# Optimization experiments

Hardware: AMD Instinct MI355X
Metric: run time of the kernel (lower is better)

The kernel has to match this reference:

```python
import jax, jax.numpy as jnp
import numpy as np
import math

FS = 9          # gaussian filter_size
STD = 1.0
LOW = 0.1       # min(threshold1, threshold2)
HIGH = 0.3      # max(threshold1, threshold2)
PAD_G = FS // 2


def _gauss_window(M, std):
    # scipy.signal.windows.gaussian: exp(-0.5*(n/std)^2), n centered, unnormalized
    n = np.arange(M, dtype=np.float64) - (M - 1) / 2.0
    return np.exp(-0.5 * (n / std) ** 2).astype(np.float32)


def _conv(x, w, pad):
    # torch F.conv2d == cross-correlation, NCHW / OIHW
    return jax.lax.conv_general_dilated(
        x, w, window_strides=(1, 1), padding=pad,
        dimension_numbers=("NCHW", "OIHW", "NCHW"))


def setup_inputs() -> dict:
    key = jax.random.key(0)
    img = jax.random.uniform(key, (8, 3, 512, 512), dtype=jnp.float32)
    g = _gauss_window(FS, STD)
    gauss_h = jnp.asarray(g[None, None, None, :])          # [1,1,1,9]
    gauss_v = jnp.asarray(g[None, None, :, None])          # [1,1,9,1]
    sobel_h = jnp.array([[[[1., 0., -1.], [2., 0., -2.], [1., 0., -1.]]]], dtype=jnp.float32)
    sobel_v = jnp.array([[[[1., 2., 1.], [0., 0., 0.], [-1., -2., -1.]]]], dtype=jnp.float32)
    d = np.zeros((8, 1, 3, 3), dtype=np.float32)
    d[:, 0, 1, 1] = 1.0
    # neighbor positions (row, col) for the -1 tap, per directional channel
    neigh = [(1, 2), (2, 2), (2, 1), (2, 0), (1, 0), (0, 0), (0, 1), (0, 2)]
    for k, (r, c) in enumerate(neigh):
        d[k, 0, r, c] = -1.0
    directional = jnp.asarray(d)                            # [8,1,3,3]
    connect = jnp.array([[[[1., 1., 1.], [1., 0., 1.], [1., 1., 1.]]]], dtype=jnp.float32)
    return {"img": img, "gauss_h": gauss_h, "gauss_v": gauss_v,
            "sobel_h": sobel_h, "sobel_v": sobel_v,
            "directional": directional, "connect": connect}


def reference(img, gauss_h, gauss_v, sobel_h, sobel_v, directional, connect):
    B, C, H, W = img.shape
    x = img.reshape(B * C, 1, H, W)  # per-channel 1-in/1-out convs, batched
    blur = _conv(_conv(x, gauss_h, [(0, 0), (PAD_G, PAD_G)]),
                 gauss_v, [(PAD_G, PAD_G), (0, 0)])
    gx = _conv(blur, sobel_h, [(1, 1), (1, 1)]).reshape(B, C, H, W)
    gy = _conv(blur, sobel_v, [(1, 1), (1, 1)]).reshape(B, C, H, W)

    # sum of per-channel magnitudes, [B,1,H,W]
    grad_mag = jnp.sqrt(gx * gx + gy * gy).sum(axis=1, keepdims=True)
    ori = jnp.arctan2(gy.sum(axis=1, keepdims=True),
                      gx.sum(axis=1, keepdims=True)) * (180.0 / math.pi) + 180.0
    ori = jnp.round(ori / 45.0) * 45.0

    all_filtered = _conv(grad_mag, directional, [(1, 1), (1, 1)])  # [B,8,H,W]

    pixel_count = B * H * W
    pr = jnp.arange(pixel_count, dtype=jnp.int32)
    flat = all_filtered.reshape(-1)
    # faithful replication of the original's flat linear-index gather
    k_pos = ((ori / 45.0) % 8.0).reshape(-1).astype(jnp.int32)
    k_neg = ((ori / 45.0 + 4.0) % 8.0).reshape(-1).astype(jnp.int32)
    pos = flat[k_pos * pixel_count + pr].reshape(B, 1, H, W)
    neg = flat[k_neg * pixel_count + pr].reshape(B, 1, H, W)

    is_max = jnp.minimum(pos, neg) > 0.0
    thin = jnp.where(is_max, grad_mag, 0.0)

    t = jnp.where(thin < LOW, 0.0, thin)
    higher = thin > HIGH
    t = jnp.where(higher, 1.0, t)
    connect_map = _conv(higher.astype(jnp.float32), connect, [(1, 1), (1, 1)])
    middle = (thin >= LOW) & (thin <= HIGH)
    t = jnp.where(middle, 0.0, t)
    connect_map = jnp.where(middle, connect_map, 0.0)
    t = jnp.where(connect_map > 0.0, 1.0, t)
    # zero borders
    t = t.at[..., 0, :].set(0.0)
    t = t.at[..., -1, :].set(0.0)
    t = t.at[..., :, 0].set(0.0)
    t = t.at[..., :, -1].set(0.0)
    return (t > 0.0).astype(jnp.float32)
```

## Files before the change

kernel.cpp:

```cpp
#include <hip/hip_runtime.h>
#include <math.h>

#define HH 512
#define WW 512
#define NB 8
#define NC 3
#define HW (HH*WW)

#define RSTRIP 16
#define CSTRIP 62
#define NROWS (HH/RSTRIP)
#define NCOLS ((WW + CSTRIP - 1)/CSTRIP)
#define WPB 2

__global__ __launch_bounds__(128) void canny_gm_kernel(
    const float* __restrict__ img, const float* __restrict__ gwin,
    float* __restrict__ GM, unsigned char* __restrict__ KP)
{
    const int lane = threadIdx.x & 63;
    const int wv   = threadIdx.x >> 6;
    const int cs   = blockIdx.x % NCOLS;
    const int rs   = (blockIdx.x / NCOLS) * WPB + wv;
    const int b    = blockIdx.y;

    const int R0 = rs * RSTRIP;
    const int cl = cs * CSTRIP - 1 + lane;

    double g[9];
#pragma unroll
    for (int k = 0; k < 9; ++k) g[k] = (double)gwin[k];

    int cidx[9]; double gk[9];
#pragma unroll
    for (int k = 0; k < 9; ++k) {
        int cc = cl - 4 + k;
        bool m = ((unsigned)cc < (unsigned)WW);
        gk[k] = m ? g[k] : 0.0;
        int cc2 = cc < 0 ? 0 : cc;
        cidx[k] = cc2 > (WW - 1) ? (WW - 1) : cc2;
    }
    const bool lane_out = (lane >= 1) && (lane <= CSTRIP) && (cl < WW);
    const bool cml = ((unsigned)(cl - 1) < (unsigned)WW);
    const bool cmr = ((unsigned)(cl + 1) < (unsigned)WW);

    const float* ip0 = img + ((size_t)b * NC + 0) * HW;
    const float* ip1 = img + ((size_t)b * NC + 1) * HW;
    const float* ip2 = img + ((size_t)b * NC + 2) * HW;

    double hb[3][9];
    double vb[3][3];
#pragma unroll
    for (int c = 0; c < 3; ++c) {
#pragma unroll
        for (int k = 0; k < 9; ++k) hb[c][k] = 0.0;
#pragma unroll
        for (int k = 0; k < 3; ++k) vb[c][k] = 0.0;
    }

    const double t225 = 0.41421356237309503;
    const double t675 = 2.414213562373095;

    auto PHASE = [&](int r, int ph, bool doV, bool doS) {
        if ((unsigned)r < (unsigned)HH) {
            const size_t ro = (size_t)r * WW;
            float v0[9], v1[9], v2[9];
#pragma unroll
            for (int k = 0; k < 9; ++k) {
                v0[k] = ip0[ro + cidx[k]];
                v1[k] = ip1[ro + cidx[k]];
                v2[k] = ip2[ro + cidx[k]];
            }
            double a0 = 0.0, a1 = 0.0, a2 = 0.0;
#pragma unroll
            for (int k = 0; k < 9; ++k) {
                a0 = fma(gk[k], (double)v0[k], a0);
                a1 = fma(gk[k], (double)v1[k], a1);
                a2 = fma(gk[k], (double)v2[k], a2);
            }
            hb[0][ph] = a0; hb[1][ph] = a1; hb[2][ph] = a2;
        } else {
            hb[0][ph] = 0.0; hb[1][ph] = 0.0; hb[2][ph] = 0.0;
        }

        if (doV) {
#pragma unroll
            for (int c = 0; c < 3; ++c) {
                double acc = 0.0;
#pragma unroll
                for (int k = 0; k < 9; ++k)
                    acc = fma(g[k], hb[c][(ph + 1 + k) % 9], acc);
                vb[c][(ph + 2) % 3] = acc;
            }
        }

        if (doS) {
            const int ri = r - 5;
            const bool up = (ri >= 1), dn = (ri <= HH - 2);
            double mag = 0.0, sgx = 0.0, sgy = 0.0;
#pragma unroll
            for (int c = 0; c < 3; ++c) {
                double top = up ? vb[c][ph % 3]       : 0.0;
                double mid =      vb[c][(ph + 1) % 3];
                double bot = dn ? vb[c][(ph + 2) % 3] : 0.0;
                double s = top + 2.0 * mid + bot;
                double d = top - bot;
                double sL = __shfl_up(s, 1), sR = __shfl_down(s, 1);
                double dL = __shfl_up(d, 1), dR = __shfl_down(d, 1);
                sL = cml ? sL : 0.0;  sR = cmr ? sR : 0.0;
                dL = cml ? dL : 0.0;  dR = cmr ? dR : 0.0;
                double gx = sL - sR;
                double gy = dL + 2.0 * d + dR;
                mag += sqrt(gx * gx + gy * gy);
                sgx += gx; sgy += gy;
            }
            if (lane_out) {
                size_t o = (size_t)b * HW + (size_t)ri * WW + cl;
                GM[o] = (float)mag;
                double ax = fabs(sgx), ay = fabs(sgy);
                int kp;
                if (ay <= ax * t225)      kp = (sgx >= 0.0) ? 4 : 0;
                else if (ay >= ax * t675) kp = (sgy > 0.0) ? 6 : 2;
                else if (sgx > 0.0)       kp = (sgy > 0.0) ? 5 : 3;
                else                      kp = (sgy > 0.0) ? 7 : 1;
                KP[o] = (unsigned char)kp;
            }
        }
    };

    {
        const int rb = R0 - 5;
#pragma unroll
        for (int ph = 0; ph < 9; ++ph) PHASE(rb + ph, ph, ph == 8, false);
    }
    {
        const int rb = R0 + 4;
#pragma unroll
        for (int ph = 0; ph < 9; ++ph) PHASE(rb + ph, ph, true, ph >= 1);
    }
    {
        const int rb = R0 + 13;
#pragma unroll
        for (int ph = 0; ph < 8; ++ph) PHASE(rb + ph, ph, true, true);
    }
}

__global__ __launch_bounds__(256) void canny_thin_out_kernel(
    const float* __restrict__ GM, const unsigned char* __restrict__ KP,
    float* __restrict__ out)
{
    __shared__ unsigned char scode[34 * 35];

    const int tilesX = WW / 32;
    const int tx0 = (blockIdx.x % tilesX) * 32;
    const int ty0 = (blockIdx.x / tilesX) * 32;
    const int b = blockIdx.y;
    const int t = threadIdx.x;

    const int dr = (int)((0x00012221u >> (b * 4)) & 15u) - 1;
    const int dc = (int)((0x21000122u >> (b * 4)) & 15u) - 1;

    {
        int r = t / 34, cc = t % 34, idx = t;
#pragma unroll
        for (int it = 0; it < 5; ++it) {
            if (idx < 34 * 34) {
                int gi = ty0 - 1 + r, gj = tx0 - 1 + cc;
                unsigned char code = 0;
                if ((unsigned)gi < (unsigned)HH && (unsigned)gj < (unsigned)WW) {
                    size_t p0 = (size_t)gi * WW + gj;
                    int kp = KP[(size_t)b * HW + p0];
                    int kn = (kp + 4) & 7;
                    int ni = gi + dr, nj = gj + dc;
                    bool nin = ((unsigned)ni < (unsigned)HH) && ((unsigned)nj < (unsigned)WW);
                    size_t pn = (size_t)ni * WW + nj;
                    double gmp  = (double)GM[(size_t)kp * HW + p0];
                    double gmn  = (double)GM[(size_t)kn * HW + p0];
                    double gmpn = nin ? (double)GM[(size_t)kp * HW + pn] : 0.0;
                    double gmnn = nin ? (double)GM[(size_t)kn * HW + pn] : 0.0;
                    double pos = gmp - gmpn;
                    double neg = gmn - gmnn;
                    double thin = (fmin(pos, neg) > 0.0) ? (double)GM[(size_t)b * HW + p0] : 0.0;
                    if (thin > 0.3) code |= 1;
                    if (thin >= 0.1 && thin <= 0.3) code |= 2;
                }
                scode[r * 35 + cc] = code;
            }
            idx += 256; r += 7; cc += 18;
            if (cc >= 34) { cc -= 34; ++r; }
        }
    }
    __syncthreads();

#pragma unroll
    for (int p = 0; p < 4; ++p) {
        int pix = t + p * 256;
        int i = pix >> 5, j = pix & 31;
        int gi = ty0 + i, gj = tx0 + j;
        float res = 0.0f;
        if (gi > 0 && gi < HH - 1 && gj > 0 && gj < WW - 1) {
            const unsigned char* sc = scode + (i + 1) * 35 + (j + 1);
            unsigned char c = *sc;
            if (c & 1) {
                res = 1.0f;
            } else if (c & 2) {
                int any = 0;
                any |= sc[-36] & 1; any |= sc[-35] & 1; any |= sc[-34] & 1;
                any |= sc[-1]  & 1; any |= sc[ 1]  & 1;
                any |= sc[ 34] & 1; any |= sc[ 35] & 1; any |= sc[ 36] & 1;
                if (any) res = 1.0f;
            }
        }
        out[(size_t)b * HW + (size_t)gi * WW + gj] = res;
    }
}

extern "C" void kernel_launch(void* const* d_in, const int* in_sizes, int n_in,
                              void* d_out, int out_size, void* d_ws, size_t ws_size,
                              hipStream_t stream) {
    const float* img  = (const float*)d_in[0];
    const float* gwin = (const float*)d_in[1];

    float* GM = (float*)d_ws;
    unsigned char* KP = (unsigned char*)d_ws + (size_t)NB * HW * sizeof(float);
    float* out = (float*)d_out;

    dim3 g1(NCOLS * (NROWS / WPB), NB);
    canny_gm_kernel<<<g1, 128, 0, stream>>>(img, gwin, GM, KP);

    dim3 g2((WW / 32) * (HH / 32), NB);
    canny_thin_out_kernel<<<g2, 256, 0, stream>>>(GM, KP, out);
}
```

Measured before the change: 70.08 us.

## Software-pipeline row loads, vectorize interior loads, shrink row strips

```diff
diff --git a/kernel.cpp b/kernel.cpp
--- a/kernel.cpp
+++ b/kernel.cpp
@@ -7,13 +7,15 @@
 #define NC 3
 #define HW (HH*WW)
 
-#define RSTRIP 16
+#define RSTRIP 8
 #define CSTRIP 62
 #define NROWS (HH/RSTRIP)
 #define NCOLS ((WW + CSTRIP - 1)/CSTRIP)
-#define WPB 2
-
-__global__ __launch_bounds__(128) void canny_gm_kernel(
+#define WPB 4
+
+typedef float float4u __attribute__((ext_vector_type(4), aligned(4)));
+
+__global__ __launch_bounds__(256) void canny_gm_kernel(
     const float* __restrict__ img, const float* __restrict__ gwin,
     float* __restrict__ GM, unsigned char* __restrict__ KP)
 {
@@ -39,6 +41,7 @@
         int cc2 = cc < 0 ? 0 : cc;
         cidx[k] = cc2 > (WW - 1) ? (WW - 1) : cc2;
     }
+    const bool csafe = (cs >= 1) && (cs <= NCOLS - 2);
     const bool lane_out = (lane >= 1) && (lane <= CSTRIP) && (cl < WW);
     const bool cml = ((unsigned)(cl - 1) < (unsigned)WW);
     const bool cmr = ((unsigned)(cl + 1) < (unsigned)WW);
@@ -60,26 +63,36 @@
     const double t225 = 0.41421356237309503;
     const double t675 = 2.414213562373095;
 
-    auto PHASE = [&](int r, int ph, bool doV, bool doS) {
-        if ((unsigned)r < (unsigned)HH) {
-            const size_t ro = (size_t)r * WW;
-            float v0[9], v1[9], v2[9];
-#pragma unroll
-            for (int k = 0; k < 9; ++k) {
-                v0[k] = ip0[ro + cidx[k]];
-                v1[k] = ip1[ro + cidx[k]];
-                v2[k] = ip2[ro + cidx[k]];
-            }
-            double a0 = 0.0, a1 = 0.0, a2 = 0.0;
-#pragma unroll
-            for (int k = 0; k < 9; ++k) {
-                a0 = fma(gk[k], (double)v0[k], a0);
-                a1 = fma(gk[k], (double)v1[k], a1);
-                a2 = fma(gk[k], (double)v2[k], a2);
-            }
-            hb[0][ph] = a0; hb[1][ph] = a1; hb[2][ph] = a2;
-        } else {
-            hb[0][ph] = 0.0; hb[1][ph] = 0.0; hb[2][ph] = 0.0;
+    auto PHASE = [&](int r, int ph, bool doLH, bool doV, bool doS) {
+        float v0[9], v1[9], v2[9];
+        if (doLH) {
+            if ((unsigned)r < (unsigned)HH) {
+                const size_t ro = (size_t)r * WW;
+                if (csafe) {
+                    const float* rp0 = ip0 + ro + (size_t)(cl - 4);
+                    const float* rp1 = ip1 + ro + (size_t)(cl - 4);
+                    const float* rp2 = ip2 + ro + (size_t)(cl - 4);
+                    float4u p0 = *(const float4u*)rp0, q0 = *(const float4u*)(rp0 + 4);
+                    float4u p1 = *(const float4u*)rp1, q1 = *(const float4u*)(rp1 + 4);
+                    float4u p2 = *(const float4u*)rp2, q2 = *(const float4u*)(rp2 + 4);
+                    v0[0]=p0[0]; v0[1]=p0[1]; v0[2]=p0[2]; v0[3]=p0[3];
+                    v0[4]=q0[0]; v0[5]=q0[1]; v0[6]=q0[2]; v0[7]=q0[3]; v0[8]=rp0[8];
+                    v1[0]=p1[0]; v1[1]=p1[1]; v1[2]=p1[2]; v1[3]=p1[3];
+                    v1[4]=q1[0]; v1[5]=q1[1]; v1[6]=q1[2]; v1[7]=q1[3]; v1[8]=rp1[8];
+                    v2[0]=p2[0]; v2[1]=p2[1]; v2[2]=p2[2]; v2[3]=p2[3];
+                    v2[4]=q2[0]; v2[5]=q2[1]; v2[6]=q2[2]; v2[7]=q2[3]; v2[8]=rp2[8];
+                } else {
+#pragma unroll
+                    for (int k = 0; k < 9; ++k) {
+                        v0[k] = ip0[ro + cidx[k]];
+                        v1[k] = ip1[ro + cidx[k]];
+                        v2[k] = ip2[ro + cidx[k]];
+                    }
+                }
+            } else {
+#pragma unroll
+                for (int k = 0; k < 9; ++k) { v0[k] = 0.0f; v1[k] = 0.0f; v2[k] = 0.0f; }
+            }
         }
 
         if (doV) {
@@ -88,20 +101,20 @@
                 double acc = 0.0;
 #pragma unroll
                 for (int k = 0; k < 9; ++k)
-                    acc = fma(g[k], hb[c][(ph + 1 + k) % 9], acc);
-                vb[c][(ph + 2) % 3] = acc;
+                    acc = fma(g[k], hb[c][(ph + k) % 9], acc);
+                vb[c][ph % 3] = acc;
             }
         }
 
         if (doS) {
-            const int ri = r - 5;
+            const int ri = r - 6;
             const bool up = (ri >= 1), dn = (ri <= HH - 2);
             double mag = 0.0, sgx = 0.0, sgy = 0.0;
 #pragma unroll
             for (int c = 0; c < 3; ++c) {
-                double top = up ? vb[c][ph % 3]       : 0.0;
-                double mid =      vb[c][(ph + 1) % 3];
-                double bot = dn ? vb[c][(ph + 2) % 3] : 0.0;
+                double top = up ? vb[c][(ph + 1) % 3] : 0.0;
+                double mid =      vb[c][(ph + 2) % 3];
+                double bot = dn ? vb[c][ph % 3]       : 0.0;
                 double s = top + 2.0 * mid + bot;
                 double d = top - bot;
                 double sL = __shfl_up(s, 1), sR = __shfl_down(s, 1);
@@ -125,22 +138,22 @@
                 KP[o] = (unsigned char)kp;
             }
         }
+
+        if (doLH) {
+#pragma unroll
+            for (int c = 0; c < 3; ++c) {
+                const float* vv = (c == 0) ? v0 : (c == 1) ? v1 : v2;
+                double a = 0.0;
+#pragma unroll
+                for (int k = 0; k < 9; ++k) a = fma(gk[k], (double)vv[k], a);
+                hb[c][ph % 9] = a;
+            }
+        }
     };
 
-    {
-        const int rb = R0 - 5;
-#pragma unroll
-        for (int ph = 0; ph < 9; ++ph) PHASE(rb + ph, ph, ph == 8, false);
-    }
-    {
-        const int rb = R0 + 4;
-#pragma unroll
-        for (int ph = 0; ph < 9; ++ph) PHASE(rb + ph, ph, true, ph >= 1);
-    }
-    {
-        const int rb = R0 + 13;
-#pragma unroll
-        for (int ph = 0; ph < 8; ++ph) PHASE(rb + ph, ph, true, true);
+#pragma unroll
+    for (int ph = 0; ph < 19; ++ph) {
+        PHASE(R0 - 5 + ph, ph, ph <= 17, ph >= 9, ph >= 11);
     }
 }
 
@@ -225,7 +238,7 @@
     float* out = (float*)d_out;
 
     dim3 g1(NCOLS * (NROWS / WPB), NB);
-    canny_gm_kernel<<<g1, 128, 0, stream>>>(img, gwin, GM, KP);
+    canny_gm_kernel<<<g1, 256, 0, stream>>>(img, gwin, GM, KP);
 
     dim3 g2((WW / 32) * (HH / 32), NB);
     canny_thin_out_kernel<<<g2, 256, 0, stream>>>(GM, KP, out);
```

Result: slower. 82.77 us (+18.1%).
